# Kernel optimization log

Measured on AMD Instinct MI355X. Metric: run time of the kernel, lower is better.

Reference implementation:

```python
import jax, jax.numpy as jnp
import numpy as np
from jax.scipy.special import logsumexp

TEMPERATURE = 0.7
N_ITERS = 8


def setup_inputs() -> dict:
    key = jax.random.key(0)
    k1, k2, k3 = jax.random.split(key, 3)
    b, n, d = 4, 8192, 1024
    num_tokens = 1024
    x = jax.random.normal(k1, (b, n, d), dtype=jnp.float32)
    routing_token = jax.random.normal(k2, (d,), dtype=jnp.float32)
    # gumbel noise: -log(-log(u)), u ~ U(0,1)
    u = jax.random.uniform(k3, (b, num_tokens, n), dtype=jnp.float32, minval=1e-20, maxval=1.0)
    gumbel = -jnp.log(jnp.clip(-jnp.log(u), 1e-20))
    mask = jnp.ones((b, n), dtype=bool)
    return {"x": x, "routing_token": routing_token, "gumbel": gumbel, "mask": mask, "num_tokens": num_tokens}


def _sinkhorn(t, n_iters=N_ITERS):
    # alternating row/col log-normalization, then exp
    def body(t, _):
        t = t - logsumexp(t, axis=-2, keepdims=True)
        t = t - logsumexp(t, axis=-1, keepdims=True)
        return t, None
    t, _ = jax.lax.scan(body, t, None, length=n_iters)
    return jnp.exp(t)


def reference(x, routing_token, gumbel, mask, num_tokens):
    b, n, d = x.shape
    mask_value = -jnp.finfo(x.dtype).max
    scores = jnp.einsum('bnd,d->bn', x, routing_token)              # [b, n]
    scores = jnp.broadcast_to(scores[:, None, :], (b, num_tokens, n))  # [b, num_tokens, n]
    smask = mask[:, None, :]                                        # [b, 1, n]
    scores = jnp.where(smask, scores, mask_value)
    # gumbel sinkhorn
    t = scores / TEMPERATURE + gumbel
    t = _sinkhorn(t)
    t = jnp.where(smask, t, mask_value)
    # topk(1) along token axis j
    selected_scores = jnp.max(t, axis=-1)                           # [b, num_tokens]
    selected_indices = jnp.argmax(t, axis=-1)                       # [b, num_tokens]
    # straight-through: forward value 1.0, gradient via selected_scores
    selected_scores = selected_scores + jax.lax.stop_gradient(1.0 - selected_scores)
    selected_mask = jnp.take_along_axis(mask, selected_indices, axis=1)
    selected_scores = jnp.where(selected_mask, selected_scores, 0.0)
    return selected_scores, selected_indices
```

## Files before the change

### kernel.cpp

```cpp
#include <hip/hip_runtime.h>
#include <math.h>

#define B 4
#define N 8192
#define K 1024
#define ROWS 8
#define KB (K / ROWS)
#define TPB 512
#define BN (B * N)

__device__ __forceinline__ void lse_step(float v, float& m, float& s) {
  float nm = fmaxf(m, v);
  s = s * __expf(m - nm) + __expf(v - nm);
  m = nm;
}
__device__ __forceinline__ void lse_merge(float m2, float s2, float& m, float& s) {
  float nm = fmaxf(m, m2);
  s = s * __expf(m - nm) + s2 * __expf(m2 - nm);
  m = nm;
}

__global__ __launch_bounds__(TPB) void col0_kernel(const float* __restrict__ g,
                                                   float* __restrict__ part) {
  int kb = blockIdx.x, b = blockIdx.y;
  const float* gbase = g + ((size_t)(b * K + kb * ROWS)) * N;
  int t = threadIdx.x;
  float cm[4][4], cs[4][4];
#pragma unroll
  for (int j = 0; j < 4; ++j)
#pragma unroll
    for (int q = 0; q < 4; ++q) { cm[j][q] = -INFINITY; cs[j][q] = 0.f; }
  for (int rI = 0; rI < ROWS; ++rI) {
    const float* gr = gbase + (size_t)rI * N;
#pragma unroll
    for (int j = 0; j < 4; ++j) {
      float4 gv = *(const float4*)(gr + j * 2048 + t * 4);
      lse_step(gv.x, cm[j][0], cs[j][0]);
      lse_step(gv.y, cm[j][1], cs[j][1]);
      lse_step(gv.z, cm[j][2], cs[j][2]);
      lse_step(gv.w, cm[j][3], cs[j][3]);
    }
  }
  float* pp = part + ((size_t)(kb * B + b)) * N;
#pragma unroll
  for (int j = 0; j < 4; ++j) {
    float4 o = make_float4(cm[j][0] + __logf(cs[j][0]), cm[j][1] + __logf(cs[j][1]),
                           cm[j][2] + __logf(cs[j][2]), cm[j][3] + __logf(cs[j][3]));
    *(float4*)(pp + j * 2048 + t * 4) = o;
  }
}

__global__ __launch_bounds__(256) void combine_kernel(const float* __restrict__ part,
                                                      float* __restrict__ d) {
  int c = threadIdx.x & 31;
  int pg = threadIdx.x >> 5;
  int idx = blockIdx.x * 32 + c;
  float m = -INFINITY, s = 0.f;
  const float* pp = part + (size_t)(pg * (KB / 8)) * BN + idx;
#pragma unroll
  for (int i = 0; i < KB / 8; ++i) lse_step(pp[(size_t)i * BN], m, s);
  __shared__ float2 red[8][32];
  red[pg][c] = make_float2(m, s);
  __syncthreads();
  if (threadIdx.x < 32) {
    float mm = red[0][threadIdx.x].x, ss = red[0][threadIdx.x].y;
#pragma unroll
    for (int w = 1; w < 8; ++w)
      lse_merge(red[w][threadIdx.x].x, red[w][threadIdx.x].y, mm, ss);
    d[blockIdx.x * 32 + threadIdx.x] = -(mm + __logf(ss));
  }
}

__global__ __launch_bounds__(TPB) void fused_kernel(const float* __restrict__ g,
                                                    const float* __restrict__ d,
                                                    float* __restrict__ part) {
  int kb = blockIdx.x, b = blockIdx.y;
  const float* gbase = g + ((size_t)(b * K + kb * ROWS)) * N;
  const float* dp = d + b * N;
  int t = threadIdx.x;
  int lane = t & 63, wv = t >> 6;

  __shared__ float2 wpart[ROWS][TPB / 64];
  __shared__ float rnew[ROWS];

  float4 dv[4];
#pragma unroll
  for (int j = 0; j < 4; ++j) dv[j] = *(const float4*)(dp + j * 2048 + t * 4);

  for (int rI = 0; rI < ROWS; ++rI) {
    const float* gr = gbase + (size_t)rI * N;
    float m0 = -INFINITY, s0 = 0.f, m1 = -INFINITY, s1 = 0.f;
    float m2 = -INFINITY, s2 = 0.f, m3 = -INFINITY, s3 = 0.f;
#pragma unroll
    for (int j = 0; j < 4; ++j) {
      float4 gv = *(const float4*)(gr + j * 2048 + t * 4);
      lse_step(gv.x + dv[j].x, m0, s0);
      lse_step(gv.y + dv[j].y, m1, s1);
      lse_step(gv.z + dv[j].z, m2, s2);
      lse_step(gv.w + dv[j].w, m3, s3);
    }
    lse_merge(m1, s1, m0, s0);
    lse_merge(m3, s3, m2, s2);
    lse_merge(m2, s2, m0, s0);
#pragma unroll
    for (int off = 32; off; off >>= 1) {
      float mm = __shfl_down(m0, off, 64);
      float ss = __shfl_down(s0, off, 64);
      lse_merge(mm, ss, m0, s0);
    }
    if (lane == 0) wpart[rI][wv] = make_float2(m0, s0);
  }
  __syncthreads();
  if (t < ROWS) {
    float m = -INFINITY, s = 0.f;
#pragma unroll
    for (int w = 0; w < TPB / 64; ++w) lse_merge(wpart[t][w].x, wpart[t][w].y, m, s);
    rnew[t] = m + __logf(s);
  }
  __syncthreads();

  float cm[4][4], cs[4][4];
#pragma unroll
  for (int j = 0; j < 4; ++j)
#pragma unroll
    for (int q = 0; q < 4; ++q) { cm[j][q] = -INFINITY; cs[j][q] = 0.f; }
  for (int rI = 0; rI < ROWS; ++rI) {
    float rk = rnew[rI];
    const float* gr = gbase + (size_t)rI * N;
#pragma unroll
    for (int j = 0; j < 4; ++j) {
      float4 gv = *(const float4*)(gr + j * 2048 + t * 4);
      lse_step(gv.x - rk, cm[j][0], cs[j][0]);
      lse_step(gv.y - rk, cm[j][1], cs[j][1]);
      lse_step(gv.z - rk, cm[j][2], cs[j][2]);
      lse_step(gv.w - rk, cm[j][3], cs[j][3]);
    }
  }
  float* pp = part + ((size_t)(kb * B + b)) * N;
#pragma unroll
  for (int j = 0; j < 4; ++j) {
    float4 o = make_float4(cm[j][0] + __logf(cs[j][0]), cm[j][1] + __logf(cs[j][1]),
                           cm[j][2] + __logf(cs[j][2]), cm[j][3] + __logf(cs[j][3]));
    *(float4*)(pp + j * 2048 + t * 4) = o;
  }
}

__global__ __launch_bounds__(256) void argmax_kernel(const float* __restrict__ g,
                                                     const float* __restrict__ d,
                                                     float* __restrict__ out) {
  int row = blockIdx.x;
  int b = row >> 10;
  const float* gp = g + (size_t)row * N;
  const float* dp = d + b * N;
  float bv = -INFINITY;
  int bi = 0;
#pragma unroll
  for (int j = 0; j < 8; ++j) {
    int n = j * 1024 + threadIdx.x * 4;
    float4 gv = *(const float4*)(gp + n);
    float4 dv = *(const float4*)(dp + n);
    float v;
    v = gv.x + dv.x; if (v > bv) { bv = v; bi = n + 0; }
    v = gv.y + dv.y; if (v > bv) { bv = v; bi = n + 1; }
    v = gv.z + dv.z; if (v > bv) { bv = v; bi = n + 2; }
    v = gv.w + dv.w; if (v > bv) { bv = v; bi = n + 3; }
  }
  __shared__ float svv[256];
  __shared__ int sii[256];
  svv[threadIdx.x] = bv;
  sii[threadIdx.x] = bi;
  __syncthreads();
  for (int off = 128; off > 0; off >>= 1) {
    if (threadIdx.x < off) {
      float v2 = svv[threadIdx.x + off];
      int i2 = sii[threadIdx.x + off];
      float v1 = svv[threadIdx.x];
      int i1 = sii[threadIdx.x];
      if (v2 > v1 || (v2 == v1 && i2 < i1)) {
        svv[threadIdx.x] = v2;
        sii[threadIdx.x] = i2;
      }
    }
    __syncthreads();
  }
  if (threadIdx.x == 0) {
    out[row] = 1.0f;
    out[B * K + row] = (float)sii[0];
  }
}

extern "C" void kernel_launch(void* const* d_in, const int* in_sizes, int n_in,
                              void* d_out, int out_size, void* d_ws, size_t ws_size,
                              hipStream_t stream) {
  const float* g = (const float*)d_in[2];
  float* out = (float*)d_out;

  char* ws = (char*)d_ws;
  float* d = (float*)ws;
  float* part = (float*)(ws + (1 << 20));

  col0_kernel<<<dim3(KB, B), TPB, 0, stream>>>(g, part);
  combine_kernel<<<BN / 32, 256, 0, stream>>>(part, d);
  for (int it = 0; it < 7; ++it) {
    fused_kernel<<<dim3(KB, B), TPB, 0, stream>>>(g, d, part);
    combine_kernel<<<BN / 32, 256, 0, stream>>>(part, d);
  }
  argmax_kernel<<<B * K, 256, 0, stream>>>(g, d, out);
}
```

Baseline: 594.6 us.

## Hold gumbel rows in registers to fuse row and column LSE in one read

The row-then-column sweep kernel now loads each group of four gumbel rows into registers once and reuses them for both the row logsumexp and the column partial logsumexp, where before each row was read twice from global memory. Blocks grow to 1024 threads covering the row with two float4s per thread, and the partial buffer layout changes to per-batch contiguous chunks, with the combine kernel indexing updated to match. Col0 and fused kernels are merged into one template. Holding 8 float4s per thread raises register pressure and may limit occupancy, and there are now two block-wide barriers per four rows.

Result: slower. 613.1 us (+3.1%).

```diff
diff --git a/kernel.cpp b/kernel.cpp
--- a/kernel.cpp
+++ b/kernel.cpp
@@ -4,10 +4,11 @@
 #define B 4
 #define N 8192
 #define K 1024
-#define ROWS 8
-#define KB (K / ROWS)
-#define TPB 512
 #define BN (B * N)
+#define RCH 8
+#define CPB (K / RCH)
+#define NCHK (B * CPB)
+#define TPA 1024
 
 __device__ __forceinline__ void lse_step(float v, float& m, float& s) {
   float nm = fmaxf(m, v);
@@ -20,45 +21,116 @@
   m = nm;
 }
 
-__global__ __launch_bounds__(TPB) void col0_kernel(const float* __restrict__ g,
-                                                   float* __restrict__ part) {
-  int kb = blockIdx.x, b = blockIdx.y;
-  const float* gbase = g + ((size_t)(b * K + kb * ROWS)) * N;
-  int t = threadIdx.x;
-  float cm[4][4], cs[4][4];
-#pragma unroll
-  for (int j = 0; j < 4; ++j)
+template <bool SUB>
+__device__ __forceinline__ void sweepA_body(const float* __restrict__ g,
+                                            const float* __restrict__ d,
+                                            float* __restrict__ part) {
+  __shared__ float2 wpart[4][16];
+  __shared__ float rns[8];
+  const int blk = blockIdx.x;
+  const int b = blk >> 7;
+  const int k0 = (blk & (CPB - 1)) * RCH;
+  const int t = threadIdx.x, lane = t & 63, wv = t >> 6;
+  const float* gbase = g + ((size_t)(b * K + k0)) * N;
+
+  float4 dv[2];
+  if (SUB) {
+#pragma unroll
+    for (int j = 0; j < 2; ++j)
+      dv[j] = *(const float4*)(d + (size_t)b * N + j * 4096 + t * 4);
+  }
+  float cm[2][4], cs[2][4];
+#pragma unroll
+  for (int j = 0; j < 2; ++j)
 #pragma unroll
     for (int q = 0; q < 4; ++q) { cm[j][q] = -INFINITY; cs[j][q] = 0.f; }
-  for (int rI = 0; rI < ROWS; ++rI) {
-    const float* gr = gbase + (size_t)rI * N;
-#pragma unroll
-    for (int j = 0; j < 4; ++j) {
-      float4 gv = *(const float4*)(gr + j * 2048 + t * 4);
-      lse_step(gv.x, cm[j][0], cs[j][0]);
-      lse_step(gv.y, cm[j][1], cs[j][1]);
-      lse_step(gv.z, cm[j][2], cs[j][2]);
-      lse_step(gv.w, cm[j][3], cs[j][3]);
+
+#pragma unroll
+  for (int sc = 0; sc < 2; ++sc) {
+    float4 gv[4][2];
+#pragma unroll
+    for (int r = 0; r < 4; ++r)
+#pragma unroll
+      for (int j = 0; j < 2; ++j)
+        gv[r][j] = *(const float4*)(gbase + (size_t)(sc * 4 + r) * N + j * 4096 + t * 4);
+    if (SUB) {
+#pragma unroll
+      for (int r = 0; r < 4; ++r) {
+        float m0 = -INFINITY, s0 = 0.f, m1 = -INFINITY, s1 = 0.f;
+        lse_step(gv[r][0].x + dv[0].x, m0, s0);
+        lse_step(gv[r][0].y + dv[0].y, m1, s1);
+        lse_step(gv[r][0].z + dv[0].z, m0, s0);
+        lse_step(gv[r][0].w + dv[0].w, m1, s1);
+        lse_step(gv[r][1].x + dv[1].x, m0, s0);
+        lse_step(gv[r][1].y + dv[1].y, m1, s1);
+        lse_step(gv[r][1].z + dv[1].z, m0, s0);
+        lse_step(gv[r][1].w + dv[1].w, m1, s1);
+        lse_merge(m1, s1, m0, s0);
+#pragma unroll
+        for (int off = 32; off; off >>= 1) {
+          float mm = __shfl_down(m0, off, 64);
+          float ss = __shfl_down(s0, off, 64);
+          lse_merge(mm, ss, m0, s0);
+        }
+        if (lane == 0) wpart[r][wv] = make_float2(m0, s0);
+      }
+      __syncthreads();
+      if (t < 64) {
+        float2 e = wpart[t >> 4][t & 15];
+        float m = e.x, s = e.y;
+#pragma unroll
+        for (int off = 1; off < 16; off <<= 1) {
+          float mm = __shfl_xor(m, off, 64);
+          float ss = __shfl_xor(s, off, 64);
+          lse_merge(mm, ss, m, s);
+        }
+        if ((t & 15) == 0) rns[sc * 4 + (t >> 4)] = m + __logf(s);
+      }
+      __syncthreads();
     }
-  }
-  float* pp = part + ((size_t)(kb * B + b)) * N;
-#pragma unroll
-  for (int j = 0; j < 4; ++j) {
+#pragma unroll
+    for (int r = 0; r < 4; ++r) {
+      float rk = SUB ? rns[sc * 4 + r] : 0.f;
+#pragma unroll
+      for (int j = 0; j < 2; ++j) {
+        lse_step(gv[r][j].x - rk, cm[j][0], cs[j][0]);
+        lse_step(gv[r][j].y - rk, cm[j][1], cs[j][1]);
+        lse_step(gv[r][j].z - rk, cm[j][2], cs[j][2]);
+        lse_step(gv[r][j].w - rk, cm[j][3], cs[j][3]);
+      }
+    }
+  }
+  float* pp = part + (size_t)blk * N;
+#pragma unroll
+  for (int j = 0; j < 2; ++j) {
     float4 o = make_float4(cm[j][0] + __logf(cs[j][0]), cm[j][1] + __logf(cs[j][1]),
                            cm[j][2] + __logf(cs[j][2]), cm[j][3] + __logf(cs[j][3]));
-    *(float4*)(pp + j * 2048 + t * 4) = o;
-  }
-}
-
-__global__ __launch_bounds__(256) void combine_kernel(const float* __restrict__ part,
-                                                      float* __restrict__ d) {
+    *(float4*)(pp + j * 4096 + t * 4) = o;
+  }
+}
+
+__global__ __launch_bounds__(TPA) void sweepA0_kernel(const float* __restrict__ g,
+                                                      const float* __restrict__ d,
+                                                      float* __restrict__ part) {
+  sweepA_body<false>(g, d, part);
+}
+__global__ __launch_bounds__(TPA) void sweepA1_kernel(const float* __restrict__ g,
+                                                      const float* __restrict__ d,
+                                                      float* __restrict__ part) {
+  sweepA_body<true>(g, d, part);
+}
+
+__global__ __launch_bounds__(256) void sweepB_kernel(const float* __restrict__ part,
+                                                     float* __restrict__ d) {
   int c = threadIdx.x & 31;
   int pg = threadIdx.x >> 5;
   int idx = blockIdx.x * 32 + c;
+  int b = idx >> 13;
+  int n = idx & (N - 1);
+  const float* pp = part + ((size_t)(b * CPB + pg * 16)) * N + n;
   float m = -INFINITY, s = 0.f;
-  const float* pp = part + (size_t)(pg * (KB / 8)) * BN + idx;
-#pragma unroll
-  for (int i = 0; i < KB / 8; ++i) lse_step(pp[(size_t)i * BN], m, s);
+#pragma unroll
+  for (int i = 0; i < 16; ++i) lse_step(pp[(size_t)i * N], m, s);
   __shared__ float2 red[8][32];
   red[pg][c] = make_float2(m, s);
   __syncthreads();
@@ -68,80 +140,6 @@
     for (int w = 1; w < 8; ++w)
       lse_merge(red[w][threadIdx.x].x, red[w][threadIdx.x].y, mm, ss);
     d[blockIdx.x * 32 + threadIdx.x] = -(mm + __logf(ss));
-  }
-}
-
-__global__ __launch_bounds__(TPB) void fused_kernel(const float* __restrict__ g,
-                                                    const float* __restrict__ d,
-                                                    float* __restrict__ part) {
-  int kb = blockIdx.x, b = blockIdx.y;
-  const float* gbase = g + ((size_t)(b * K + kb * ROWS)) * N;
-  const float* dp = d + b * N;
-  int t = threadIdx.x;
-  int lane = t & 63, wv = t >> 6;
-
-  __shared__ float2 wpart[ROWS][TPB / 64];
-  __shared__ float rnew[ROWS];
-
-  float4 dv[4];
-#pragma unroll
-  for (int j = 0; j < 4; ++j) dv[j] = *(const float4*)(dp + j * 2048 + t * 4);
-
-  for (int rI = 0; rI < ROWS; ++rI) {
-    const float* gr = gbase + (size_t)rI * N;
-    float m0 = -INFINITY, s0 = 0.f, m1 = -INFINITY, s1 = 0.f;
-    float m2 = -INFINITY, s2 = 0.f, m3 = -INFINITY, s3 = 0.f;
-#pragma unroll
-    for (int j = 0; j < 4; ++j) {
-      float4 gv = *(const float4*)(gr + j * 2048 + t * 4);
-      lse_step(gv.x + dv[j].x, m0, s0);
-      lse_step(gv.y + dv[j].y, m1, s1);
-      lse_step(gv.z + dv[j].z, m2, s2);
-      lse_step(gv.w + dv[j].w, m3, s3);
-    }
-    lse_merge(m1, s1, m0, s0);
-    lse_merge(m3, s3, m2, s2);
-    lse_merge(m2, s2, m0, s0);
-#pragma unroll
-    for (int off = 32; off; off >>= 1) {
-      float mm = __shfl_down(m0, off, 64);
-      float ss = __shfl_down(s0, off, 64);
-      lse_merge(mm, ss, m0, s0);
-    }
-    if (lane == 0) wpart[rI][wv] = make_float2(m0, s0);
-  }
-  __syncthreads();
-  if (t < ROWS) {
-    float m = -INFINITY, s = 0.f;
-#pragma unroll
-    for (int w = 0; w < TPB / 64; ++w) lse_merge(wpart[t][w].x, wpart[t][w].y, m, s);
-    rnew[t] = m + __logf(s);
-  }
-  __syncthreads();
-
-  float cm[4][4], cs[4][4];
-#pragma unroll
-  for (int j = 0; j < 4; ++j)
-#pragma unroll
-    for (int q = 0; q < 4; ++q) { cm[j][q] = -INFINITY; cs[j][q] = 0.f; }
-  for (int rI = 0; rI < ROWS; ++rI) {
-    float rk = rnew[rI];
-    const float* gr = gbase + (size_t)rI * N;
-#pragma unroll
-    for (int j = 0; j < 4; ++j) {
-      float4 gv = *(const float4*)(gr + j * 2048 + t * 4);
-      lse_step(gv.x - rk, cm[j][0], cs[j][0]);
-      lse_step(gv.y - rk, cm[j][1], cs[j][1]);
-      lse_step(gv.z - rk, cm[j][2], cs[j][2]);
-      lse_step(gv.w - rk, cm[j][3], cs[j][3]);
-    }
-  }
-  float* pp = part + ((size_t)(kb * B + b)) * N;
-#pragma unroll
-  for (int j = 0; j < 4; ++j) {
-    float4 o = make_float4(cm[j][0] + __logf(cs[j][0]), cm[j][1] + __logf(cs[j][1]),
-                           cm[j][2] + __logf(cs[j][2]), cm[j][3] + __logf(cs[j][3]));
-    *(float4*)(pp + j * 2048 + t * 4) = o;
   }
 }
 
@@ -199,11 +197,11 @@
   float* d = (float*)ws;
   float* part = (float*)(ws + (1 << 20));
 
-  col0_kernel<<<dim3(KB, B), TPB, 0, stream>>>(g, part);
-  combine_kernel<<<BN / 32, 256, 0, stream>>>(part, d);
+  sweepA0_kernel<<<NCHK, TPA, 0, stream>>>(g, d, part);
+  sweepB_kernel<<<BN / 32, 256, 0, stream>>>(part, d);
   for (int it = 0; it < 7; ++it) {
-    fused_kernel<<<dim3(KB, B), TPB, 0, stream>>>(g, d, part);
-    combine_kernel<<<BN / 32, 256, 0, stream>>>(part, d);
+    sweepA1_kernel<<<NCHK, TPA, 0, stream>>>(g, d, part);
+    sweepB_kernel<<<BN / 32, 256, 0, stream>>>(part, d);
   }
   argmax_kernel<<<B * K, 256, 0, stream>>>(g, d, out);
 }
```
